# Kernel optimization log

Measured on AMD Instinct MI355X. Metric: run time of the kernel, lower is better.

## Reference

```python
import jax, jax.numpy as jnp
import numpy as np

N_GRAPHS = 256      # graphs in the batch
N_PER = 52          # nodes per peptide graph (module default num_nodes=52)
IN_CH = 21          # amino-acid one-hot features
HIDDEN = 128
OUT_EG = 128
LATENT = 64
N_LAYERS = 4


def _fc_edges(n_graphs, n_per):
    """Block-diagonal fully-connected directed edges (no self loops)."""
    base = np.arange(n_per)
    r, c = np.meshgrid(base, base, indexing='ij')
    mask = r != c
    r, c = r[mask], c[mask]                       # [n_per*(n_per-1)]
    offs = (np.arange(n_graphs) * n_per)[:, None]
    row = (r[None, :] + offs).reshape(-1)
    col = (c[None, :] + offs).reshape(-1)
    return row.astype(np.int32), col.astype(np.int32)


def setup_inputs() -> dict:
    key = jax.random.key(0)
    ks = iter(jax.random.split(key, 40))

    def rn(shape, scale=0.05):
        return jax.random.normal(next(ks), shape, dtype=jnp.float32) * scale

    N = N_GRAPHS * N_PER
    row, col = _fc_edges(N_GRAPHS, N_PER)
    L, H = N_LAYERS, HIDDEN
    return {
        'x': jax.random.normal(next(ks), (N, IN_CH), dtype=jnp.float32),
        'pos': jax.random.normal(next(ks), (N, 3), dtype=jnp.float32),
        'edge_row': jnp.asarray(row),
        'edge_col': jnp.asarray(col),
        'batch': jnp.repeat(jnp.arange(N_GRAPHS, dtype=jnp.int32), N_PER),
        'emb_in_w': rn((IN_CH, H)), 'emb_in_b': jnp.zeros((H,), jnp.float32),
        'edge_w1': rn((L, 2 * H + 1, H)), 'edge_b1': jnp.zeros((L, H), jnp.float32),
        'edge_w2': rn((L, H, H)), 'edge_b2': jnp.zeros((L, H), jnp.float32),
        'node_w1': rn((L, 2 * H, H)), 'node_b1': jnp.zeros((L, H), jnp.float32),
        'node_w2': rn((L, H, H)), 'node_b2': jnp.zeros((L, H), jnp.float32),
        'coord_w1': rn((L, H, H)), 'coord_b1': jnp.zeros((L, H), jnp.float32),
        'coord_w2': rn((L, H, 1), scale=0.001),   # xavier gain=0.001, no bias
        'emb_out_w': rn((H, OUT_EG)), 'emb_out_b': jnp.zeros((OUT_EG,), jnp.float32),
        'mean_w': rn((OUT_EG, LATENT)), 'mean_b': jnp.zeros((LATENT,), jnp.float32),
        'logvar_w': rn((OUT_EG, LATENT)), 'logvar_b': jnp.zeros((LATENT,), jnp.float32),
    }


def _segment_mean(data, ids, n):
    s = jax.ops.segment_sum(data, ids, num_segments=n)
    cnt = jax.ops.segment_sum(jnp.ones((data.shape[0],), data.dtype), ids, num_segments=n)
    return s / jnp.clip(cnt, 1.0)[:, None]


def _egcl(h, coord, row, col, p):
    """One E_GCL layer (residual=True, coords_agg='mean', no attention/tanh/normalize)."""
    ew1, eb1, ew2, eb2, nw1, nb1, nw2, nb2, cw1, cb1, cw2 = p
    n = h.shape[0]
    coord_diff = coord[row] - coord[col]                     # [E,3]
    radial = jnp.sum(coord_diff * coord_diff, axis=1, keepdims=True)  # [E,1]
    # edge model
    m = jnp.concatenate([h[row], h[col], radial], axis=1)    # [E,2H+1]
    m = jax.nn.silu(m @ ew1 + eb1)
    edge_feat = jax.nn.silu(m @ ew2 + eb2)                   # [E,H]
    # coord model: per-edge scalar, mean-aggregated onto source nodes
    t = jax.nn.silu(edge_feat @ cw1 + cb1) @ cw2             # [E,1]
    coord = coord + _segment_mean(coord_diff * t, row, n)
    # node model: sum-aggregate edge features, MLP, residual
    agg = jax.ops.segment_sum(edge_feat, row, num_segments=n)
    z = jnp.concatenate([h, agg], axis=1)                    # [N,2H]
    z = jax.nn.silu(z @ nw1 + nb1)
    h = h + (z @ nw2 + nb2)
    return h, coord


def reference(x, pos, edge_row, edge_col, batch,
              emb_in_w, emb_in_b,
              edge_w1, edge_b1, edge_w2, edge_b2,
              node_w1, node_b1, node_w2, node_b2,
              coord_w1, coord_b1, coord_w2,
              emb_out_w, emb_out_b,
              mean_w, mean_b, logvar_w, logvar_b):
    h = x @ emb_in_w + emb_in_b
    coord = pos
    for i in range(edge_w1.shape[0]):
        h, coord = _egcl(h, coord, edge_row, edge_col,
                         (edge_w1[i], edge_b1[i], edge_w2[i], edge_b2[i],
                          node_w1[i], node_b1[i], node_w2[i], node_b2[i],
                          coord_w1[i], coord_b1[i], coord_w2[i]))
    h = h @ emb_out_w + emb_out_b                            # embedding_out
    g = _segment_mean(h, batch, N_GRAPHS)                    # global_mean_pool
    mean = g @ mean_w + mean_b
    log_var = g @ logvar_w + logvar_b
    return mean, log_var
```

## Files before the change

### kernel.cpp

```cpp
#include <hip/hip_runtime.h>

constexpr int NPER = 52;
constexpr int HID  = 128;
constexpr int INCH = 21;
constexpr int NLAY = 4;
constexpr int LATD = 64;
constexpr int NGRAPH = 256;
constexpr int TPB  = 1024;
constexpr int TSTR = 424;
constexpr int TILE = 16 * TSTR;

typedef short short8 __attribute__((ext_vector_type(8)));
typedef float f32x4  __attribute__((ext_vector_type(4)));

constexpr int W1T_OFF = 0;
constexpr int W1T_SZ  = NLAY * 256 * HID;
constexpr int W2T_OFF = W1T_OFF + W1T_SZ;
constexpr int W2T_SZ  = NLAY * HID * HID;
constexpr int C1T_OFF = W2T_OFF + W2T_SZ;
constexpr int C1T_SZ  = NLAY * HID * HID;
constexpr int N1T_OFF = C1T_OFF + C1T_SZ;
constexpr int N1T_SZ  = NLAY * HID * 2 * HID;
constexpr int N2T_OFF = N1T_OFF + N1T_SZ;
constexpr int N2T_SZ  = NLAY * HID * HID;
constexpr int WS_ELEMS = N2T_OFF + N2T_SZ;

__device__ __forceinline__ unsigned cvt_pk_bf16(float a, float b) {
    unsigned r;
    asm("v_cvt_pk_bf16_f32 %0, %1, %2" : "=v"(r) : "v"(a), "v"(b));
    return r;
}
__device__ __forceinline__ unsigned short f2bf(float f) {
    return (unsigned short)cvt_pk_bf16(f, f);
}
__device__ __forceinline__ float bf2f(unsigned short h) {
    return __uint_as_float(((unsigned)h) << 16);
}
__device__ __forceinline__ float fast_rcp(float x) {
    float r;
    asm("v_rcp_f32 %0, %1" : "=v"(r) : "v"(x));
    return r;
}
__device__ __forceinline__ float silu_f(float v) {
    return v * fast_rcp(1.0f + __expf(-v));
}
__device__ __forceinline__ f32x4 mfma16(short8 a, short8 b, f32x4 c) {
    return __builtin_amdgcn_mfma_f32_16x16x32_bf16(a, b, c, 0, 0, 0);
}

__device__ __forceinline__ int tidx(int row, int e) {
    return (e >> 3) * TSTR + row * 8 + (e & 7);
}

__global__ void conv_w(const float* __restrict__ ew1, const float* __restrict__ ew2,
                       const float* __restrict__ cw1, const float* __restrict__ nw1,
                       const float* __restrict__ nw2, unsigned short* __restrict__ ws)
{
    int idx = blockIdx.x * 256 + threadIdx.x;
    if (idx >= WS_ELEMS) return;
    float v;
    if (idx < W2T_OFF) {
        int t = idx - W1T_OFF;
        int L = t / (256 * HID), rem = t % (256 * HID);
        int n = rem / HID, k = rem % HID;
        v = (n < HID) ? ew1[(size_t)L * 257 * HID + k * HID + n]
                      : ew1[(size_t)L * 257 * HID + (HID + k) * HID + (n - HID)];
    } else if (idx < C1T_OFF) {
        int t = idx - W2T_OFF;
        int L = t / (HID * HID), rem = t % (HID * HID);
        int n = rem / HID, k = rem % HID;
        v = ew2[(size_t)L * HID * HID + k * HID + n];
    } else if (idx < N1T_OFF) {
        int t = idx - C1T_OFF;
        int L = t / (HID * HID), rem = t % (HID * HID);
        int n = rem / HID, k = rem % HID;
        v = cw1[(size_t)L * HID * HID + k * HID + n];
    } else if (idx < N2T_OFF) {
        int t = idx - N1T_OFF;
        int L = t / (HID * 2 * HID), rem = t % (HID * 2 * HID);
        int n = rem / (2 * HID), k = rem % (2 * HID);
        v = nw1[(size_t)L * 2 * HID * HID + k * HID + n];
    } else {
        int t = idx - N2T_OFF;
        int L = t / (HID * HID), rem = t % (HID * HID);
        int n = rem / HID, k = rem % HID;
        v = nw2[(size_t)L * HID * HID + k * HID + n];
    }
    ws[idx] = f2bf(v);
}

constexpr int LDS_FLOATS = 1024 + 156 + 156 + 128 + 512 + 128;
constexpr size_t SHMEM_BYTES = (size_t)8 * TILE * 2 + LDS_FLOATS * 4;

__device__ __forceinline__ void coord_agg(int r, int rr, const float* tpart,
                                          const float* coord_s, float* cacc_s, int lane)
{
    float dx = 0.f, dy = 0.f, dz = 0.f;
    if (lane < NPER) {
        const float* tb = tpart + rr * 256;
        float tc = tb[lane] + tb[64 + lane] + tb[128 + lane] + tb[192 + lane];
        dx = (coord_s[r * 3 + 0] - coord_s[lane * 3 + 0]) * tc;
        dy = (coord_s[r * 3 + 1] - coord_s[lane * 3 + 1]) * tc;
        dz = (coord_s[r * 3 + 2] - coord_s[lane * 3 + 2]) * tc;
    }
    #pragma unroll
    for (int m = 1; m < 64; m <<= 1) {
        dx += __shfl_xor(dx, m); dy += __shfl_xor(dy, m); dz += __shfl_xor(dz, m);
    }
    if (lane == 0) {
        cacc_s[r * 3 + 0] = dx; cacc_s[r * 3 + 1] = dy; cacc_s[r * 3 + 2] = dz;
    }
}

extern "C" __global__ void __launch_bounds__(TPB, 4)
egnn_mfma(const float* __restrict__ x, const float* __restrict__ pos,
          const float* __restrict__ emb_in_w, const float* __restrict__ emb_in_b,
          const float* __restrict__ edge_w1,
          const float* __restrict__ edge_b1, const float* __restrict__ edge_b2,
          const float* __restrict__ node_b1, const float* __restrict__ node_b2,
          const float* __restrict__ coord_b1, const float* __restrict__ coord_w2,
          const float* __restrict__ emb_out_w, const float* __restrict__ emb_out_b,
          const float* __restrict__ mean_w, const float* __restrict__ mean_b,
          const float* __restrict__ logvar_w, const float* __restrict__ logvar_b,
          const unsigned short* __restrict__ ws, float* __restrict__ out)
{
    extern __shared__ __align__(16) char smem[];
    unsigned short* m0_t = (unsigned short*)smem;
    unsigned short* m1_t = m0_t + TILE;
    unsigned short* e0_t = m1_t + TILE;
    unsigned short* e1_t = e0_t + TILE;
    unsigned short* h_t  = e1_t + TILE;
    unsigned short* ag_t = h_t  + TILE;
    unsigned short* A_t  = ag_t + TILE;
    unsigned short* B_t  = A_t  + TILE;
    float* aggp    = (float*)(B_t + TILE);
    float* coord_s = aggp + 1024;
    float* cacc_s  = coord_s + 156;
    float* rad_s   = cacc_s + 156;
    float* tpart   = rad_s + 128;
    float* wr_s    = tpart + 512;

    const int g    = blockIdx.x;
    const int tid  = threadIdx.x;
    const int lane = tid & 63;
    const int wv   = tid >> 6;
    const int mp   = wv >> 2;
    const int np   = wv & 3;
    const int l15  = lane & 15;
    const int kb   = lane >> 4;
    const int rowA = mp * 16 + l15;
    const int crow0 = mp * 16 + kb * 4;
    const int n0   = 32 * np + l15;
    const int n1   = n0 + 16;
    const int jp   = 2 * lane;
    const int pb   = (jp >> 3) * TSTR + (jp & 7);
    const int fo   = kb * TSTR + rowA * 8;

    {
        float* xs = (float*)m0_t;
        for (int p = tid; p < NPER * INCH; p += TPB) xs[p] = x[(size_t)g * NPER * INCH + p];
        for (int p = tid; p < NPER * 3; p += TPB)    coord_s[p] = pos[(size_t)g * NPER * 3 + p];
    }
    __syncthreads();

    for (int p = tid; p < NPER * HID; p += TPB) {
        int c = p >> 7, j = p & 127;
        float s = emb_in_b[j];
        #pragma unroll 7
        for (int k = 0; k < INCH; ++k) s += ((float*)m0_t)[c * INCH + k] * emb_in_w[k * HID + j];
        h_t[tidx(c, j)] = f2bf(s);
    }
    __syncthreads();

    for (int L = 0; L < NLAY; ++L) {
        const unsigned short* w1t = ws + W1T_OFF + (size_t)L * 256 * HID;
        const unsigned short* w2t = ws + W2T_OFF + (size_t)L * HID * HID;
        const unsigned short* c1t = ws + C1T_OFF + (size_t)L * HID * HID;
        const unsigned short* n1t = ws + N1T_OFF + (size_t)L * HID * 2 * HID;
        const unsigned short* n2t = ws + N2T_OFF + (size_t)L * HID * HID;

        short8 wE[8], wC[8];
        #pragma unroll
        for (int s = 0; s < 4; ++s) {
            wE[s]     = *(const short8*)(w2t + (size_t)n0 * HID + 32 * s + 8 * kb);
            wE[4 + s] = *(const short8*)(w2t + (size_t)n1 * HID + 32 * s + 8 * kb);
            wC[s]     = *(const short8*)(c1t + (size_t)n0 * HID + 32 * s + 8 * kb);
            wC[4 + s] = *(const short8*)(c1t + (size_t)n1 * HID + 32 * s + 8 * kb);
        }
        float eb2v[2], cb1v[2], cw2v[2];
        eb2v[0] = edge_b2[L * HID + n0];  eb2v[1] = edge_b2[L * HID + n1];
        cb1v[0] = coord_b1[L * HID + n0]; cb1v[1] = coord_b1[L * HID + n1];
        cw2v[0] = coord_w2[L * HID + n0]; cw2v[1] = coord_w2[L * HID + n1];
        if (tid < HID) wr_s[tid] = edge_w1[(size_t)L * 257 * HID + 256 * HID + tid];

        {
            f32x4 acc[4];
            #pragma unroll
            for (int q = 0; q < 4; ++q) acc[q] = (f32x4){0.f, 0.f, 0.f, 0.f};
            #pragma unroll
            for (int s = 0; s < 4; ++s) {
                short8 af = *(const short8*)(h_t + fo + s * 4 * TSTR);
                #pragma unroll
                for (int q = 0; q < 4; ++q) {
                    int n = l15 + 16 * (4 * np + q);
                    short8 bf = *(const short8*)(w1t + (size_t)n * HID + 32 * s + 8 * kb);
                    acc[q] = mfma16(af, bf, acc[q]);
                }
            }
            #pragma unroll
            for (int q = 0; q < 4; ++q) {
                int n = l15 + 16 * (4 * np + q);
                float eb1 = (n < HID) ? edge_b1[L * HID + n] : 0.f;
                #pragma unroll
                for (int reg = 0; reg < 4; ++reg) {
                    int c = crow0 + reg;
                    if (c < NPER) {
                        float v = acc[q][reg] + eb1;
                        if (n < HID) A_t[tidx(c, n)] = f2bf(v);
                        else         B_t[tidx(c, n - HID)] = f2bf(v);
                    }
                }
            }
        }
        if (tid < NPER) {
            float dx = coord_s[0] - coord_s[tid * 3 + 0];
            float dy = coord_s[1] - coord_s[tid * 3 + 1];
            float dz = coord_s[2] - coord_s[tid * 3 + 2];
            rad_s[tid] = dx * dx + dy * dy + dz * dz;
        } else if (tid >= 64 && tid < 64 + NPER) {
            int c = tid - 64;
            float dx = coord_s[3] - coord_s[c * 3 + 0];
            float dy = coord_s[4] - coord_s[c * 3 + 1];
            float dz = coord_s[5] - coord_s[c * 3 + 2];
            rad_s[64 + c] = dx * dx + dy * dy + dz * dz;
        }
        __syncthreads();

        const float wrl = wr_s[jp], wrh = wr_s[jp + 1];

        for (int gp = 0; gp < 26; ++gp) {
            const int r0 = 2 * gp, r1 = r0 + 1;

            {
                unsigned pa0 = *(const unsigned*)(A_t + pb + r0 * 8);
                unsigned pa1 = *(const unsigned*)(A_t + pb + r1 * 8);
                float A0l = bf2f((unsigned short)(pa0 & 0xffff)), A0h = bf2f((unsigned short)(pa0 >> 16));
                float A1l = bf2f((unsigned short)(pa1 & 0xffff)), A1h = bf2f((unsigned short)(pa1 >> 16));
                for (int j = wv; j < 2 * NPER; j += 16) {
                    int rr = (j >= NPER);
                    int c  = rr ? j - NPER : j;
                    float Al = rr ? A1l : A0l, Ah = rr ? A1h : A0h;
                    float rad = rad_s[rr * 64 + c];
                    unsigned bp = *(const unsigned*)(B_t + pb + c * 8);
                    float v0 = Al + bf2f((unsigned short)(bp & 0xffff)) + rad * wrl;
                    float v1 = Ah + bf2f((unsigned short)(bp >> 16))    + rad * wrh;
                    unsigned mv = cvt_pk_bf16(silu_f(v0), silu_f(v1));
                    *(unsigned*)((rr ? m1_t : m0_t) + pb + c * 8) = mv;
                }
            }
            __syncthreads();

            {
                f32x4 e00 = (f32x4){0.f,0.f,0.f,0.f}, e01 = e00, e10 = e00, e11 = e00;
                #pragma unroll
                for (int s = 0; s < 4; ++s) {
                    short8 af0 = *(const short8*)(m0_t + fo + s * 4 * TSTR);
                    short8 af1 = *(const short8*)(m1_t + fo + s * 4 * TSTR);
                    e00 = mfma16(af0, wE[s], e00); e01 = mfma16(af0, wE[4 + s], e01);
                    e10 = mfma16(af1, wE[s], e10); e11 = mfma16(af1, wE[4 + s], e11);
                }
                #pragma unroll
                for (int rr = 0; rr < 2; ++rr) {
                    f32x4 ea = rr ? e10 : e00, eb = rr ? e11 : e01;
                    unsigned short* et = rr ? e1_t : e0_t;
                    const int r = rr ? r1 : r0;
                    float a0 = 0.f, a1 = 0.f;
                    #pragma unroll
                    for (int reg = 0; reg < 4; ++reg) {
                        int c = crow0 + reg;
                        float v0 = silu_f(ea[reg] + eb2v[0]);
                        float v1 = silu_f(eb[reg] + eb2v[1]);
                        if (c < NPER) {
                            et[tidx(c, n0)] = f2bf(v0);
                            et[tidx(c, n1)] = f2bf(v1);
                            if (c != r) { a0 += v0; a1 += v1; }
                        }
                    }
                    a0 += __shfl_xor(a0, 16); a0 += __shfl_xor(a0, 32);
                    a1 += __shfl_xor(a1, 16); a1 += __shfl_xor(a1, 32);
                    if (kb == 0) {
                        float* ar = aggp + (rr * 4 + mp) * HID;
                        ar[n0] = a0; ar[n1] = a1;
                    }
                }
                if (wv < 2 && gp > 0) coord_agg(2 * gp - 2 + wv, wv, tpart, coord_s, cacc_s, lane);
            }
            __syncthreads();

            {
                f32x4 y00 = (f32x4){0.f,0.f,0.f,0.f}, y01 = y00, y10 = y00, y11 = y00;
                #pragma unroll
                for (int s = 0; s < 4; ++s) {
                    short8 af0 = *(const short8*)(e0_t + fo + s * 4 * TSTR);
                    short8 af1 = *(const short8*)(e1_t + fo + s * 4 * TSTR);
                    y00 = mfma16(af0, wC[s], y00); y01 = mfma16(af0, wC[4 + s], y01);
                    y10 = mfma16(af1, wC[s], y10); y11 = mfma16(af1, wC[4 + s], y11);
                }
                #pragma unroll
                for (int rr = 0; rr < 2; ++rr) {
                    f32x4 ya = rr ? y10 : y00, yb = rr ? y11 : y01;
                    float* tp = tpart + (rr * 4 + np) * 64;
                    #pragma unroll
                    for (int reg = 0; reg < 4; ++reg) {
                        float v = silu_f(ya[reg] + cb1v[0]) * cw2v[0]
                                + silu_f(yb[reg] + cb1v[1]) * cw2v[1];
                        v += __shfl_xor(v, 1); v += __shfl_xor(v, 2);
                        v += __shfl_xor(v, 4); v += __shfl_xor(v, 8);
                        if (l15 == 0) tp[crow0 + reg] = v;
                    }
                }
            }
            if (tid < 256) {
                int rr = tid >> 7, t = tid & 127;
                const float* ap = aggp + rr * 512;
                float a = ap[t] + ap[128 + t] + ap[256 + t] + ap[384 + t];
                ag_t[tidx(2 * gp + rr, t)] = f2bf(a);
            } else if (tid < 384 && gp + 1 < 26) {
                int t = tid - 256, rr = t >> 6, c = t & 63;
                if (c < NPER) {
                    int r = 2 * (gp + 1) + rr;
                    float dx = coord_s[r * 3 + 0] - coord_s[c * 3 + 0];
                    float dy = coord_s[r * 3 + 1] - coord_s[c * 3 + 1];
                    float dz = coord_s[r * 3 + 2] - coord_s[c * 3 + 2];
                    rad_s[rr * 64 + c] = dx * dx + dy * dy + dz * dz;
                }
            }
            __syncthreads();
        }

        if (wv < 2) coord_agg(50 + wv, wv, tpart, coord_s, cacc_s, lane);
        {
            float nb1v[2];
            nb1v[0] = node_b1[L * HID + n0]; nb1v[1] = node_b1[L * HID + n1];
            f32x4 z0 = (f32x4){0.f,0.f,0.f,0.f}, z1 = z0;
            #pragma unroll
            for (int s = 0; s < 4; ++s) {
                short8 af = *(const short8*)(h_t + fo + s * 4 * TSTR);
                z0 = mfma16(af, *(const short8*)(n1t + (size_t)n0 * 2 * HID + 32 * s + 8 * kb), z0);
                z1 = mfma16(af, *(const short8*)(n1t + (size_t)n1 * 2 * HID + 32 * s + 8 * kb), z1);
            }
            #pragma unroll
            for (int s = 0; s < 4; ++s) {
                short8 af = *(const short8*)(ag_t + fo + s * 4 * TSTR);
                z0 = mfma16(af, *(const short8*)(n1t + (size_t)n0 * 2 * HID + HID + 32 * s + 8 * kb), z0);
                z1 = mfma16(af, *(const short8*)(n1t + (size_t)n1 * 2 * HID + HID + 32 * s + 8 * kb), z1);
            }
            #pragma unroll
            for (int reg = 0; reg < 4; ++reg) {
                int c = crow0 + reg;
                if (c < NPER) {
                    m0_t[tidx(c, n0)] = f2bf(silu_f(z0[reg] + nb1v[0]));
                    m0_t[tidx(c, n1)] = f2bf(silu_f(z1[reg] + nb1v[1]));
                }
            }
        }
        __syncthreads();

        if (tid < NPER * 3) coord_s[tid] += cacc_s[tid] * (1.0f / 51.0f);
        {
            float nb2v[2];
            nb2v[0] = node_b2[L * HID + n0]; nb2v[1] = node_b2[L * HID + n1];
            f32x4 d0 = (f32x4){0.f,0.f,0.f,0.f}, d1 = d0;
            #pragma unroll
            for (int s = 0; s < 4; ++s) {
                short8 af = *(const short8*)(m0_t + fo + s * 4 * TSTR);
                d0 = mfma16(af, *(const short8*)(n2t + (size_t)n0 * HID + 32 * s + 8 * kb), d0);
                d1 = mfma16(af, *(const short8*)(n2t + (size_t)n1 * HID + 32 * s + 8 * kb), d1);
            }
            #pragma unroll
            for (int reg = 0; reg < 4; ++reg) {
                int c = crow0 + reg;
                if (c < NPER) {
                    int i0 = tidx(c, n0), i1 = tidx(c, n1);
                    h_t[i0] = f2bf(bf2f(h_t[i0]) + d0[reg] + nb2v[0]);
                    h_t[i1] = f2bf(bf2f(h_t[i1]) + d1[reg] + nb2v[1]);
                }
            }
        }
        __syncthreads();
    }

    float* gm = aggp;
    float* eg = aggp + HID;
    if (tid < HID) {
        float s = 0.f;
        for (int c = 0; c < NPER; ++c) s += bf2f(h_t[tidx(c, tid)]);
        gm[tid] = s * (1.0f / 52.0f);
    }
    __syncthreads();
    if (tid < HID) {
        float s = emb_out_b[tid];
        #pragma unroll 4
        for (int k = 0; k < HID; ++k) s += gm[k] * emb_out_w[k * HID + tid];
        eg[tid] = s;
    }
    __syncthreads();
    if (tid < 2 * LATD) {
        const int  l   = tid & (LATD - 1);
        const bool ism = tid < LATD;
        const float* W = ism ? mean_w : logvar_w;
        float s = ism ? mean_b[l] : logvar_b[l];
        #pragma unroll 4
        for (int k = 0; k < HID; ++k) s += eg[k] * W[k * LATD + l];
        out[(ism ? 0 : NGRAPH * LATD) + g * LATD + l] = s;
    }
}

extern "C" void kernel_launch(void* const* d_in, const int* in_sizes, int n_in,
                              void* d_out, int out_size, void* d_ws, size_t ws_size,
                              hipStream_t stream) {
    const float* x         = (const float*)d_in[0];
    const float* pos       = (const float*)d_in[1];
    const float* emb_in_w  = (const float*)d_in[5];
    const float* emb_in_b  = (const float*)d_in[6];
    const float* edge_w1   = (const float*)d_in[7];
    const float* edge_b1   = (const float*)d_in[8];
    const float* edge_w2   = (const float*)d_in[9];
    const float* edge_b2   = (const float*)d_in[10];
    const float* node_w1   = (const float*)d_in[11];
    const float* node_b1   = (const float*)d_in[12];
    const float* node_w2   = (const float*)d_in[13];
    const float* node_b2   = (const float*)d_in[14];
    const float* coord_w1  = (const float*)d_in[15];
    const float* coord_b1  = (const float*)d_in[16];
    const float* coord_w2  = (const float*)d_in[17];
    const float* emb_out_w = (const float*)d_in[18];
    const float* emb_out_b = (const float*)d_in[19];
    const float* mean_w    = (const float*)d_in[20];
    const float* mean_b    = (const float*)d_in[21];
    const float* logvar_w  = (const float*)d_in[22];
    const float* logvar_b  = (const float*)d_in[23];

    unsigned short* ws = (unsigned short*)d_ws;

    conv_w<<<(WS_ELEMS + 255) / 256, 256, 0, stream>>>(edge_w1, edge_w2, coord_w1,
                                                       node_w1, node_w2, ws);

    (void)hipFuncSetAttribute(reinterpret_cast<const void*>(egnn_mfma),
                              hipFuncAttributeMaxDynamicSharedMemorySize,
                              (int)SHMEM_BYTES);

    hipLaunchKernelGGL(egnn_mfma, dim3(NGRAPH), dim3(TPB), SHMEM_BYTES, stream,
                       x, pos, emb_in_w, emb_in_b, edge_w1,
                       edge_b1, edge_b2, node_b1, node_b2,
                       coord_b1, coord_w2, emb_out_w, emb_out_b,
                       mean_w, mean_b, logvar_w, logvar_b,
                       ws, (float*)d_out);
}
```

Baseline: 806.2 us.

## Software-pipeline edge message build into coord phase, removing one barrier per step

```diff
diff --git a/kernel.cpp b/kernel.cpp
--- a/kernel.cpp
+++ b/kernel.cpp
@@ -36,17 +36,18 @@
 __device__ __forceinline__ float bf2f(unsigned short h) {
     return __uint_as_float(((unsigned)h) << 16);
 }
-__device__ __forceinline__ float fast_rcp(float x) {
-    float r;
-    asm("v_rcp_f32 %0, %1" : "=v"(r) : "v"(x));
-    return r;
-}
+__device__ __forceinline__ float blo(unsigned u) { return __uint_as_float(u << 16); }
+__device__ __forceinline__ float bhi(unsigned u) { return __uint_as_float(u & 0xffff0000u); }
 __device__ __forceinline__ float silu_f(float v) {
-    return v * fast_rcp(1.0f + __expf(-v));
+    float e, r;
+    asm("v_exp_f32 %0, %1" : "=v"(e) : "v"(v * -1.44269504088896341f));
+    asm("v_rcp_f32 %0, %1" : "=v"(r) : "v"(1.0f + e));
+    return v * r;
 }
 __device__ __forceinline__ f32x4 mfma16(short8 a, short8 b, f32x4 c) {
     return __builtin_amdgcn_mfma_f32_16x16x32_bf16(a, b, c, 0, 0, 0);
 }
+__device__ __forceinline__ short8 as_s8(f32x4 v) { return __builtin_bit_cast(short8, v); }
 
 __device__ __forceinline__ int tidx(int row, int e) {
     return (e >> 3) * TSTR + row * 8 + (e & 7);
@@ -89,7 +90,7 @@
     ws[idx] = f2bf(v);
 }
 
-constexpr int LDS_FLOATS = 1024 + 156 + 156 + 128 + 512 + 128;
+constexpr int LDS_FLOATS = 1024 + 156 + 156 + 256 + 512 + 128;
 constexpr size_t SHMEM_BYTES = (size_t)8 * TILE * 2 + LDS_FLOATS * 4;
 
 __device__ __forceinline__ void coord_agg(int r, int rr, const float* tpart,
@@ -109,6 +110,38 @@
     }
     if (lane == 0) {
         cacc_s[r * 3 + 0] = dx; cacc_s[r * 3 + 1] = dy; cacc_s[r * 3 + 2] = dz;
+    }
+}
+
+__device__ __forceinline__ void mstep(int p, const unsigned short* A_t, const unsigned short* B_t,
+                                      unsigned short* m0_t, unsigned short* m1_t,
+                                      const float* rad_s,
+                                      float w40, float w41, float w42, float w43,
+                                      int pb4, int wv, int half)
+{
+    if (wv >= 12) return;
+    const float* radp = rad_s + (p & 1) * 128;
+    uint2 a0 = *(const uint2*)(A_t + pb4 + (2 * p) * 8);
+    uint2 a1 = *(const uint2*)(A_t + pb4 + (2 * p + 1) * 8);
+    float A00 = blo(a0.x), A01 = bhi(a0.x), A02 = blo(a0.y), A03 = bhi(a0.y);
+    float A10 = blo(a1.x), A11 = bhi(a1.x), A12 = blo(a1.y), A13 = bhi(a1.y);
+    #pragma unroll
+    for (int i = 0; i < 5; ++i) {
+        int u = wv + 12 * i;
+        if (u < 52) {
+            int rr = (u >= 26) ? 1 : 0;
+            int c = 2 * (u - 26 * rr) + half;
+            float rad = radp[rr * 64 + c];
+            uint2 b = *(const uint2*)(B_t + pb4 + c * 8);
+            float v0 = (rr ? A10 : A00) + blo(b.x) + rad * w40;
+            float v1 = (rr ? A11 : A01) + bhi(b.x) + rad * w41;
+            float v2 = (rr ? A12 : A02) + blo(b.y) + rad * w42;
+            float v3 = (rr ? A13 : A03) + bhi(b.y) + rad * w43;
+            uint2 o;
+            o.x = cvt_pk_bf16(silu_f(v0), silu_f(v1));
+            o.y = cvt_pk_bf16(silu_f(v2), silu_f(v3));
+            *(uint2*)((rr ? m1_t : m0_t) + pb4 + c * 8) = o;
+        }
     }
 }
 
@@ -137,7 +170,7 @@
     float* coord_s = aggp + 1024;
     float* cacc_s  = coord_s + 156;
     float* rad_s   = cacc_s + 156;
-    float* tpart   = rad_s + 128;
+    float* tpart   = rad_s + 256;
     float* wr_s    = tpart + 512;
 
     const int g    = blockIdx.x;
@@ -152,8 +185,11 @@
     const int crow0 = mp * 16 + kb * 4;
     const int n0   = 32 * np + l15;
     const int n1   = n0 + 16;
-    const int jp   = 2 * lane;
-    const int pb   = (jp >> 3) * TSTR + (jp & 7);
+    const int eb0  = (n0 >> 3) * TSTR + (n0 & 7);
+    const int eb1x = (n1 >> 3) * TSTR + (n1 & 7);
+    const int half = lane >> 5;
+    const int col4 = (lane & 31) * 4;
+    const int pb4  = (col4 >> 3) * TSTR + (col4 & 7);
     const int fo   = kb * TSTR + rowA * 8;
 
     {
@@ -179,18 +215,23 @@
         const unsigned short* n1t = ws + N1T_OFF + (size_t)L * HID * 2 * HID;
         const unsigned short* n2t = ws + N2T_OFF + (size_t)L * HID * HID;
 
-        short8 wE[8], wC[8];
+        f32x4 wE[8], wC[8];
         #pragma unroll
         for (int s = 0; s < 4; ++s) {
-            wE[s]     = *(const short8*)(w2t + (size_t)n0 * HID + 32 * s + 8 * kb);
-            wE[4 + s] = *(const short8*)(w2t + (size_t)n1 * HID + 32 * s + 8 * kb);
-            wC[s]     = *(const short8*)(c1t + (size_t)n0 * HID + 32 * s + 8 * kb);
-            wC[4 + s] = *(const short8*)(c1t + (size_t)n1 * HID + 32 * s + 8 * kb);
-        }
+            wE[s]     = __builtin_bit_cast(f32x4, *(const short8*)(w2t + (size_t)n0 * HID + 32 * s + 8 * kb));
+            wE[4 + s] = __builtin_bit_cast(f32x4, *(const short8*)(w2t + (size_t)n1 * HID + 32 * s + 8 * kb));
+            wC[s]     = __builtin_bit_cast(f32x4, *(const short8*)(c1t + (size_t)n0 * HID + 32 * s + 8 * kb));
+            wC[4 + s] = __builtin_bit_cast(f32x4, *(const short8*)(c1t + (size_t)n1 * HID + 32 * s + 8 * kb));
+        }
+        #pragma unroll
+        for (int s = 0; s < 8; ++s) asm volatile("" : "+v"(wE[s]), "+v"(wC[s]));
+
         float eb2v[2], cb1v[2], cw2v[2];
         eb2v[0] = edge_b2[L * HID + n0];  eb2v[1] = edge_b2[L * HID + n1];
         cb1v[0] = coord_b1[L * HID + n0]; cb1v[1] = coord_b1[L * HID + n1];
         cw2v[0] = coord_w2[L * HID + n0]; cw2v[1] = coord_w2[L * HID + n1];
+        asm volatile("" : "+v"(eb2v[0]), "+v"(eb2v[1]), "+v"(cb1v[0]), "+v"(cb1v[1]),
+                          "+v"(cw2v[0]), "+v"(cw2v[1]));
         if (tid < HID) wr_s[tid] = edge_w1[(size_t)L * 257 * HID + 256 * HID + tid];
 
         {
@@ -222,43 +263,27 @@
                 }
             }
         }
-        if (tid < NPER) {
-            float dx = coord_s[0] - coord_s[tid * 3 + 0];
-            float dy = coord_s[1] - coord_s[tid * 3 + 1];
-            float dz = coord_s[2] - coord_s[tid * 3 + 2];
-            rad_s[tid] = dx * dx + dy * dy + dz * dz;
-        } else if (tid >= 64 && tid < 64 + NPER) {
-            int c = tid - 64;
-            float dx = coord_s[3] - coord_s[c * 3 + 0];
-            float dy = coord_s[4] - coord_s[c * 3 + 1];
-            float dz = coord_s[5] - coord_s[c * 3 + 2];
-            rad_s[64 + c] = dx * dx + dy * dy + dz * dz;
+        if (wv < 4 && lane < NPER) {
+            int r = wv;
+            float dx = coord_s[r * 3 + 0] - coord_s[lane * 3 + 0];
+            float dy = coord_s[r * 3 + 1] - coord_s[lane * 3 + 1];
+            float dz = coord_s[r * 3 + 2] - coord_s[lane * 3 + 2];
+            rad_s[(r >> 1) * 128 + (r & 1) * 64 + lane] = dx * dx + dy * dy + dz * dz;
         }
         __syncthreads();
 
-        const float wrl = wr_s[jp], wrh = wr_s[jp + 1];
+        float w40, w41, w42, w43;
+        {
+            float4 w4 = *(const float4*)(wr_s + col4);
+            w40 = w4.x; w41 = w4.y; w42 = w4.z; w43 = w4.w;
+            asm volatile("" : "+v"(w40), "+v"(w41), "+v"(w42), "+v"(w43));
+        }
+
+        mstep(0, A_t, B_t, m0_t, m1_t, rad_s, w40, w41, w42, w43, pb4, wv, half);
+        __syncthreads();
 
         for (int gp = 0; gp < 26; ++gp) {
             const int r0 = 2 * gp, r1 = r0 + 1;
-
-            {
-                unsigned pa0 = *(const unsigned*)(A_t + pb + r0 * 8);
-                unsigned pa1 = *(const unsigned*)(A_t + pb + r1 * 8);
-                float A0l = bf2f((unsigned short)(pa0 & 0xffff)), A0h = bf2f((unsigned short)(pa0 >> 16));
-                float A1l = bf2f((unsigned short)(pa1 & 0xffff)), A1h = bf2f((unsigned short)(pa1 >> 16));
-                for (int j = wv; j < 2 * NPER; j += 16) {
-                    int rr = (j >= NPER);
-                    int c  = rr ? j - NPER : j;
-                    float Al = rr ? A1l : A0l, Ah = rr ? A1h : A0h;
-                    float rad = rad_s[rr * 64 + c];
-                    unsigned bp = *(const unsigned*)(B_t + pb + c * 8);
-                    float v0 = Al + bf2f((unsigned short)(bp & 0xffff)) + rad * wrl;
-                    float v1 = Ah + bf2f((unsigned short)(bp >> 16))    + rad * wrh;
-                    unsigned mv = cvt_pk_bf16(silu_f(v0), silu_f(v1));
-                    *(unsigned*)((rr ? m1_t : m0_t) + pb + c * 8) = mv;
-                }
-            }
-            __syncthreads();
 
             {
                 f32x4 e00 = (f32x4){0.f,0.f,0.f,0.f}, e01 = e00, e10 = e00, e11 = e00;
@@ -266,8 +291,8 @@
                 for (int s = 0; s < 4; ++s) {
                     short8 af0 = *(const short8*)(m0_t + fo + s * 4 * TSTR);
                     short8 af1 = *(const short8*)(m1_t + fo + s * 4 * TSTR);
-                    e00 = mfma16(af0, wE[s], e00); e01 = mfma16(af0, wE[4 + s], e01);
-                    e10 = mfma16(af1, wE[s], e10); e11 = mfma16(af1, wE[4 + s], e11);
+                    e00 = mfma16(af0, as_s8(wE[s]), e00); e01 = mfma16(af0, as_s8(wE[4 + s]), e01);
+                    e10 = mfma16(af1, as_s8(wE[s]), e10); e11 = mfma16(af1, as_s8(wE[4 + s]), e11);
                 }
                 #pragma unroll
                 for (int rr = 0; rr < 2; ++rr) {
@@ -281,8 +306,8 @@
                         float v0 = silu_f(ea[reg] + eb2v[0]);
                         float v1 = silu_f(eb[reg] + eb2v[1]);
                         if (c < NPER) {
-                            et[tidx(c, n0)] = f2bf(v0);
-                            et[tidx(c, n1)] = f2bf(v1);
+                            et[eb0 + c * 8] = f2bf(v0);
+                            et[eb1x + c * 8] = f2bf(v1);
                             if (c != r) { a0 += v0; a1 += v1; }
                         }
                     }
@@ -293,7 +318,7 @@
                         ar[n0] = a0; ar[n1] = a1;
                     }
                 }
-                if (wv < 2 && gp > 0) coord_agg(2 * gp - 2 + wv, wv, tpart, coord_s, cacc_s, lane);
+                if (wv < 2 && gp > 0) coord_agg(2 * (gp - 1) + wv, wv, tpart, coord_s, cacc_s, lane);
             }
             __syncthreads();
 
@@ -303,8 +328,8 @@
                 for (int s = 0; s < 4; ++s) {
                     short8 af0 = *(const short8*)(e0_t + fo + s * 4 * TSTR);
                     short8 af1 = *(const short8*)(e1_t + fo + s * 4 * TSTR);
-                    y00 = mfma16(af0, wC[s], y00); y01 = mfma16(af0, wC[4 + s], y01);
-                    y10 = mfma16(af1, wC[s], y10); y11 = mfma16(af1, wC[4 + s], y11);
+                    y00 = mfma16(af0, as_s8(wC[s]), y00); y01 = mfma16(af0, as_s8(wC[4 + s]), y01);
+                    y10 = mfma16(af1, as_s8(wC[s]), y10); y11 = mfma16(af1, as_s8(wC[4 + s]), y11);
                 }
                 #pragma unroll
                 for (int rr = 0; rr < 2; ++rr) {
@@ -320,25 +345,35 @@
                     }
                 }
             }
-            if (tid < 256) {
-                int rr = tid >> 7, t = tid & 127;
-                const float* ap = aggp + rr * 512;
-                float a = ap[t] + ap[128 + t] + ap[256 + t] + ap[384 + t];
-                ag_t[tidx(2 * gp + rr, t)] = f2bf(a);
-            } else if (tid < 384 && gp + 1 < 26) {
-                int t = tid - 256, rr = t >> 6, c = t & 63;
-                if (c < NPER) {
-                    int r = 2 * (gp + 1) + rr;
-                    float dx = coord_s[r * 3 + 0] - coord_s[c * 3 + 0];
-                    float dy = coord_s[r * 3 + 1] - coord_s[c * 3 + 1];
-                    float dz = coord_s[r * 3 + 2] - coord_s[c * 3 + 2];
-                    rad_s[rr * 64 + c] = dx * dx + dy * dy + dz * dz;
+            if (gp + 1 < 26)
+                mstep(gp + 1, A_t, B_t, m0_t, m1_t, rad_s, w40, w41, w42, w43, pb4, wv, half);
+            if (wv >= 14) {
+                if (gp + 2 < 26) {
+                    int t3 = (wv - 14) * 64 + lane;
+                    int rr = t3 >> 6, c = t3 & 63;
+                    if (c < NPER) {
+                        int r = 2 * (gp + 2) + rr;
+                        float dx = coord_s[r * 3 + 0] - coord_s[c * 3 + 0];
+                        float dy = coord_s[r * 3 + 1] - coord_s[c * 3 + 1];
+                        float dz = coord_s[r * 3 + 2] - coord_s[c * 3 + 2];
+                        rad_s[(gp & 1) * 128 + rr * 64 + c] = dx * dx + dy * dy + dz * dz;
+                    }
+                }
+            } else if (wv >= 12) {
+                #pragma unroll
+                for (int q = 0; q < 2; ++q) {
+                    int t2 = (wv - 12) * 128 + q * 64 + lane;
+                    int rr = t2 >> 7, t = t2 & 127;
+                    const float* ap = aggp + rr * 512;
+                    float a = ap[t] + ap[128 + t] + ap[256 + t] + ap[384 + t];
+                    ag_t[(t >> 3) * TSTR + (2 * gp + rr) * 8 + (t & 7)] = f2bf(a);
                 }
             }
             __syncthreads();
         }
 
         if (wv < 2) coord_agg(50 + wv, wv, tpart, coord_s, cacc_s, lane);
+
         {
             float nb1v[2];
             nb1v[0] = node_b1[L * HID + n0]; nb1v[1] = node_b1[L * HID + n1];
```

New measurement: 813.0 us. About the same (+0.8%).
